# Performance work log

Measured on AMD Instinct MI355X. Metric: run time of the kernel, lower is better.

The kernel has to match this reference:

```python
import jax, jax.numpy as jnp
import numpy as np

T, B, DIM, N_STATE = 2048, 16, 1024, 1024
EPS = 1e-6


def setup_inputs() -> dict:
    key = jax.random.key(0)
    kx, kk, kv, kq = jax.random.split(key, 4)
    xavier = np.sqrt(2.0 / (N_STATE + DIM)).astype(np.float32)
    return {
        "x": jax.random.normal(kx, (T, B, DIM), dtype=jnp.float32),
        "W_k": jax.random.normal(kk, (N_STATE, DIM), dtype=jnp.float32) * xavier,
        "W_v": jax.random.normal(kv, (N_STATE, DIM), dtype=jnp.float32) * xavier,
        "W_q": jax.random.normal(kq, (N_STATE, DIM), dtype=jnp.float32) * xavier,
    }


def reference(x, W_k, W_v, W_q):
    # Projections for all timesteps at once: [T, B, n]
    k = jnp.einsum("tbd,nd->tbn", x, W_k)
    v = jnp.einsum("tbd,nd->tbn", x, W_v)
    q = jnp.einsum("tbd,nd->tbn", x, W_q)
    # L2-normalize k per (t, b) over the state dim (matches k_t.norm(dim=-1))
    k_norm = k / (jnp.linalg.norm(k, axis=-1, keepdims=True) + EPS)

    Tn, Bn, n = k.shape
    S0 = jnp.zeros((Bn, n), dtype=x.dtype)

    def step(S, inp):
        k_t, v_t, q_t = inp
        # Delta update with OUTPUT gating + tanh nonlinearity
        S_new = jnp.tanh(S * (1.0 - k_t * k_t) + v_t * k_t)
        Sq = S_new * q_t
        out = Sq * jax.nn.silu(Sq)
        return S_new, out

    S_final, output = jax.lax.scan(step, S0, (k_norm, v, q))
    return output, S_final
```

## Files before the change

### kernel.cpp

```cpp
#include <hip/hip_runtime.h>
#include <hip/hip_fp16.h>

#define T_STEPS 2048
#define BATCH 16
#define DIMD 1024
#define NSTATE 1024
#define MROWS (T_STEPS * BATCH)
#define NCH (BATCH * NSTATE)

typedef _Float16 f16x8 __attribute__((ext_vector_type(8)));
typedef float f32x4 __attribute__((ext_vector_type(4)));

#define GAS(p) ((const __attribute__((address_space(1))) void*)(p))
#define LAS(p) ((__attribute__((address_space(3))) void*)(p))

__global__ void cvt_kernel(const float* __restrict__ src, _Float16* __restrict__ dst, int n8) {
  int i = blockIdx.x * blockDim.x + threadIdx.x;
  if (i >= n8) return;
  const float4* s4 = (const float4*)src;
  float4 a = s4[(size_t)i * 2];
  float4 b = s4[(size_t)i * 2 + 1];
  f16x8 o;
  o[0] = (_Float16)a.x; o[1] = (_Float16)a.y; o[2] = (_Float16)a.z; o[3] = (_Float16)a.w;
  o[4] = (_Float16)b.x; o[5] = (_Float16)b.y; o[6] = (_Float16)b.z; o[7] = (_Float16)b.w;
  *((f16x8*)dst + i) = o;
}

__global__ void cvtW_kernel(const float* __restrict__ wk, const float* __restrict__ wv,
                            const float* __restrict__ wq, _Float16* __restrict__ dst) {
  const float* src = blockIdx.y == 0 ? wk : blockIdx.y == 1 ? wv : wq;
  int i = blockIdx.x * blockDim.x + threadIdx.x;
  const float4* s4 = (const float4*)src;
  float4 a = s4[(size_t)i * 2];
  float4 b = s4[(size_t)i * 2 + 1];
  f16x8 o;
  o[0] = (_Float16)a.x; o[1] = (_Float16)a.y; o[2] = (_Float16)a.z; o[3] = (_Float16)a.w;
  o[4] = (_Float16)b.x; o[5] = (_Float16)b.y; o[6] = (_Float16)b.z; o[7] = (_Float16)b.w;
  *((f16x8*)dst + (size_t)blockIdx.y * (NSTATE * DIMD / 8) + i) = o;
}

__global__ __launch_bounds__(512, 1) void gemm_kernel(const _Float16* __restrict__ A,
                                                      const _Float16* __restrict__ Wcat,
                                                      _Float16* __restrict__ KVQt,
                                                      float* __restrict__ rnpart) {
  __shared__ _Float16 lds[65536];
  const int tid = threadIdx.x;
  const int lane = tid & 63;
  const int w = tid >> 6;
  const int wm = w >> 2;
  const int wn = w & 3;

  const int bid = blockIdx.x;
  const int swz = (bid & 7) * 192 + (bid >> 3);
  const int mat = swz >> 9;
  const int rem = swz & 511;
  const int tileM = rem >> 2;
  const int tileN = rem & 3;

  const _Float16* Ag = A + (size_t)tileM * 256 * DIMD;
  const _Float16* Bg = Wcat + (size_t)mat * NSTATE * DIMD + (size_t)tileN * 256 * DIMD;

  const int s0 = tid, s1 = tid + 512;
  const int sr0 = s0 >> 2, sc0 = ((s0 & 3) ^ ((s0 >> 3) & 3)) * 8;
  const int sr1 = s1 >> 2, sc1 = ((s1 & 3) ^ ((s1 >> 3) & 3)) * 8;

#define STAGE_H(G, buf, reg, TT, h)                                                     \
  do {                                                                                  \
    __builtin_amdgcn_global_load_lds(                                                   \
        GAS(G + (size_t)sr0 * DIMD + (TT) * 64 + (h) * 32 + sc0),                       \
        LAS(lds + (buf) * 32768 + (reg) * 8192 + s0 * 8), 16, 0, 0);                    \
    __builtin_amdgcn_global_load_lds(                                                   \
        GAS(G + (size_t)sr1 * DIMD + (TT) * 64 + (h) * 32 + sc1),                       \
        LAS(lds + (buf) * 32768 + (reg) * 8192 + s1 * 8), 16, 0, 0);                    \
  } while (0)

  f32x4 acc[8][4];
#pragma unroll
  for (int m = 0; m < 8; ++m)
#pragma unroll
    for (int n = 0; n < 4; ++n)
      acc[m][n] = (f32x4){0.f, 0.f, 0.f, 0.f};

  STAGE_H(Ag, 0, 0, 0, 0);
  STAGE_H(Bg, 0, 2, 0, 0);
  STAGE_H(Ag, 0, 1, 0, 1);
  STAGE_H(Bg, 0, 3, 0, 1);

  const int fr = lane & 15;
  const int cbp = ((lane >> 4) ^ ((fr >> 1) & 3)) * 8;

#define KTILE(T)                                                                        \
  do {                                                                                  \
    const int buf = (T) & 1, bufn = buf ^ 1;                                            \
    f16x8 a0[8], b0[4], a1[8], b1[4];                                                   \
                 \
    asm volatile("s_waitcnt vmcnt(4)" ::: "memory");                                    \
    __builtin_amdgcn_s_barrier();                                                       \
    __builtin_amdgcn_sched_barrier(0);                                                  \
    if ((T) + 1 < 16) STAGE_H(Ag, bufn, 0, (T) + 1, 0);                                 \
    _Pragma("unroll") for (int m = 0; m < 8; ++m)                                       \
        a0[m] = *(const f16x8*)(lds + buf * 32768 + 0 * 8192 +                          \
                                (wm * 128 + m * 16 + fr) * 32 + cbp);                   \
    _Pragma("unroll") for (int n = 0; n < 4; ++n)                                       \
        b0[n] = *(const f16x8*)(lds + buf * 32768 + 2 * 8192 +                          \
                                (wn * 64 + n * 16 + fr) * 32 + cbp);                    \
    __builtin_amdgcn_s_setprio(1);                                                      \
    _Pragma("unroll") for (int m = 0; m < 8; ++m) _Pragma("unroll") for (int n = 0; n < 2; ++n) \
        acc[m][n] = __builtin_amdgcn_mfma_f32_16x16x32_f16(a0[m], b0[n], acc[m][n], 0, 0, 0); \
    __builtin_amdgcn_s_setprio(0);                                                      \
                                         \
    if ((T) + 1 < 16) STAGE_H(Bg, bufn, 2, (T) + 1, 0);                                 \
    __builtin_amdgcn_s_setprio(1);                                                      \
    _Pragma("unroll") for (int m = 0; m < 8; ++m) _Pragma("unroll") for (int n = 2; n < 4; ++n) \
        acc[m][n] = __builtin_amdgcn_mfma_f32_16x16x32_f16(a0[m], b0[n], acc[m][n], 0, 0, 0); \
    __builtin_amdgcn_s_setprio(0);                                                      \
                  \
    if ((T) + 1 < 16) {                                                                 \
      asm volatile("s_waitcnt vmcnt(4)" ::: "memory");                                  \
    } else {                                                                            \
      asm volatile("s_waitcnt vmcnt(0)" ::: "memory");                                  \
    }                                                                                   \
    __builtin_amdgcn_s_barrier();                                                       \
    __builtin_amdgcn_sched_barrier(0);                                                  \
    if ((T) + 1 < 16) STAGE_H(Ag, bufn, 1, (T) + 1, 1);                                 \
    _Pragma("unroll") for (int m = 0; m < 8; ++m)                                       \
        a1[m] = *(const f16x8*)(lds + buf * 32768 + 1 * 8192 +                          \
                                (wm * 128 + m * 16 + fr) * 32 + cbp);                   \
    _Pragma("unroll") for (int n = 0; n < 4; ++n)                                       \
        b1[n] = *(const f16x8*)(lds + buf * 32768 + 3 * 8192 +                          \
                                (wn * 64 + n * 16 + fr) * 32 + cbp);                    \
    __builtin_amdgcn_s_setprio(1);                                                      \
    _Pragma("unroll") for (int m = 0; m < 8; ++m) _Pragma("unroll") for (int n = 0; n < 2; ++n) \
        acc[m][n] = __builtin_amdgcn_mfma_f32_16x16x32_f16(a1[m], b1[n], acc[m][n], 0, 0, 0); \
    __builtin_amdgcn_s_setprio(0);                                                      \
                                         \
    if ((T) + 1 < 16) STAGE_H(Bg, bufn, 3, (T) + 1, 1);                                 \
    __builtin_amdgcn_s_setprio(1);                                                      \
    _Pragma("unroll") for (int m = 0; m < 8; ++m) _Pragma("unroll") for (int n = 2; n < 4; ++n) \
        acc[m][n] = __builtin_amdgcn_mfma_f32_16x16x32_f16(a1[m], b1[n], acc[m][n], 0, 0, 0); \
    __builtin_amdgcn_s_setprio(0);                                                      \
  } while (0)

  KTILE(0);  KTILE(1);  KTILE(2);  KTILE(3);
  KTILE(4);  KTILE(5);  KTILE(6);  KTILE(7);
  KTILE(8);  KTILE(9);  KTILE(10); KTILE(11);
  KTILE(12); KTILE(13); KTILE(14); KTILE(15);

  const int cc = lane & 15;
  const int l4 = lane >> 4;
  _Float16* Cb = KVQt + (size_t)mat * ((size_t)MROWS * NSTATE) +
                 (size_t)(tileM * 2 + wm) * ((size_t)NCH * 8);
#pragma unroll
  for (int n = 0; n < 4; ++n)
#pragma unroll
    for (int j = 0; j < 4; ++j) {
      f16x8 pk;
#pragma unroll
      for (int m = 0; m < 8; ++m) pk[m] = (_Float16)acc[m][n][j];
      const int b = l4 * 4 + j;
      const int gcol = tileN * 256 + wn * 64 + n * 16 + cc;
      *(f16x8*)(Cb + ((size_t)(b * 1024 + gcol)) * 8) = pk;
    }

  if (mat == 0) {
#pragma unroll
    for (int m = 0; m < 8; ++m)
#pragma unroll
      for (int j = 0; j < 4; ++j) {
        float p = 0.f;
#pragma unroll
        for (int n = 0; n < 4; ++n) p += acc[m][n][j] * acc[m][n][j];
        p += __shfl_xor(p, 1);
        p += __shfl_xor(p, 2);
        p += __shfl_xor(p, 4);
        p += __shfl_xor(p, 8);
        if (cc == 0) {
          const int gr = tileM * 256 + wm * 128 + m * 16 + l4 * 4 + j;
          rnpart[(size_t)(tileN * 4 + wn) * MROWS + gr] = p;
        }
      }
  }
}

__global__ void rnfin_kernel(const float* __restrict__ part, float* __restrict__ rnT) {
  const int r = blockIdx.x * 256 + threadIdx.x;
  float s = 0.f;
#pragma unroll
  for (int i = 0; i < 16; ++i) s += part[(size_t)i * MROWS + r];
  rnT[(r & 15) * T_STEPS + (r >> 4)] = 1.f / (sqrtf(s) + 1e-6f);
}

#define STILE 16

#define LOADT(P, t0in)                                                        \
  do {                                                                        \
    const int tc = ((t0in) < T_STEPS) ? (t0in) : (T_STEPS - STILE);           \
    const size_t o0 = ((size_t)(tc >> 3) * NCH + c) * 8;                      \
    P##k0 = *(const f16x8*)(Kt + o0);                                         \
    P##k1 = *(const f16x8*)(Kt + o0 + (size_t)NCH * 8);                       \
    P##v0 = *(const f16x8*)(Vt + o0);                                         \
    P##v1 = *(const f16x8*)(Vt + o0 + (size_t)NCH * 8);                       \
    P##q0 = *(const f16x8*)(Qt + o0);                                         \
    P##q1 = *(const f16x8*)(Qt + o0 + (size_t)NCH * 8);                       \
    P##r0 = *(const f32x4*)(rnT + bb + tc);                                   \
    P##r1 = *(const f32x4*)(rnT + bb + tc + 4);                               \
    P##r2 = *(const f32x4*)(rnT + bb + tc + 8);                               \
    P##r3 = *(const f32x4*)(rnT + bb + tc + 12);                              \
  } while (0)

#define STEPT(P, t0)                                                          \
  do {                                                                        \
    float a2[STILE], b2[STILE], qf[STILE];                                    \
    _Pragma("unroll") for (int i = 0; i < STILE; ++i) {                       \
      float kf = (float)((i < 8) ? P##k0[i & 7] : P##k1[i & 7]);              \
      float vf = (float)((i < 8) ? P##v0[i & 7] : P##v1[i & 7]);              \
      float rv = (i < 4) ? P##r0[i & 3]                                       \
               : (i < 8) ? P##r1[i & 3]                                       \
               : (i < 12) ? P##r2[i & 3] : P##r3[i & 3];                      \
      float kn = kf * rv;                                                     \
      a2[i] = L2E2 - (L2E2 * kn) * kn;                                        \
      b2[i] = L2E2 * (vf * kn);                                               \
      qf[i] = (float)((i < 8) ? P##q0[i & 7] : P##q1[i & 7]);                 \
    }                                                                         \
    _Pragma("unroll") for (int i = 0; i < STILE; ++i) {                       \
      float u = fmaf(S, a2[i], b2[i]);                                        \
      float e = __builtin_amdgcn_exp2f(u);                                    \
      float r = __builtin_amdgcn_rcpf(e + 1.f);                               \
      S = fmaf(-2.f, r, 1.f);                                                 \
      float z = S * qf[i];                                                    \
      float sg = __builtin_amdgcn_rcpf(1.f + __builtin_amdgcn_exp2f(-L2E * z)); \
      out[(size_t)((t0) + i) * NCH + c] = z * z * sg;                         \
    }                                                                         \
  } while (0)

__global__ __launch_bounds__(64) void scan_kernel(const _Float16* __restrict__ Kt,
                                                  const _Float16* __restrict__ Vt,
                                                  const _Float16* __restrict__ Qt,
                                                  const float* __restrict__ rnT,
                                                  float* __restrict__ out,
                                                  float* __restrict__ sfin) {
  const int c = blockIdx.x * 64 + threadIdx.x;
  const int bb = (c >> 10) * T_STEPS;
  constexpr float L2E2 = 2.8853900817779268f;
  constexpr float L2E = 1.4426950408889634f;
  float S = 0.f;
  f16x8 Ak0, Ak1, Av0, Av1, Aq0, Aq1;
  f16x8 Bk0, Bk1, Bv0, Bv1, Bq0, Bq1;
  f16x8 Ck0, Ck1, Cv0, Cv1, Cq0, Cq1;
  f16x8 Dk0, Dk1, Dv0, Dv1, Dq0, Dq1;
  f32x4 Ar0, Ar1, Ar2, Ar3, Br0, Br1, Br2, Br3;
  f32x4 Cr0, Cr1, Cr2, Cr3, Dr0, Dr1, Dr2, Dr3;

  LOADT(A, 0);
  LOADT(B, STILE);
  LOADT(C, 2 * STILE);
  for (int t0 = 0; t0 < T_STEPS; t0 += 4 * STILE) {
    LOADT(D, t0 + 3 * STILE);
    STEPT(A, t0);
    LOADT(A, t0 + 4 * STILE);
    STEPT(B, t0 + STILE);
    LOADT(B, t0 + 5 * STILE);
    STEPT(C, t0 + 2 * STILE);
    LOADT(C, t0 + 6 * STILE);
    STEPT(D, t0 + 3 * STILE);
  }
  sfin[c] = S;
}

extern "C" void kernel_launch(void* const* d_in, const int* in_sizes, int n_in,
                              void* d_out, int out_size, void* d_ws, size_t ws_size,
                              hipStream_t stream) {
  const float* x = (const float*)d_in[0];
  const float* Wk = (const float*)d_in[1];
  const float* Wv = (const float*)d_in[2];
  const float* Wq = (const float*)d_in[3];

  char* ws = (char*)d_ws;
  _Float16* xh = (_Float16*)ws;
  _Float16* Wh = (_Float16*)(ws + 67108864ull);
  _Float16* KVQt = (_Float16*)(ws + 67108864ull + 6291456ull);
  float* rnpart = (float*)(ws + 67108864ull + 6291456ull + 201326592ull);
  float* rnT = (float*)(ws + 67108864ull + 6291456ull + 201326592ull + 2097152ull);

  int n8x = MROWS * DIMD / 8;
  cvt_kernel<<<(n8x + 255) / 256, 256, 0, stream>>>(x, xh, n8x);
  cvtW_kernel<<<dim3(NSTATE * DIMD / 8 / 256, 3), 256, 0, stream>>>(Wk, Wv, Wq, Wh);

  gemm_kernel<<<1536, 512, 0, stream>>>(xh, Wh, KVQt, rnpart);

  rnfin_kernel<<<MROWS / 256, 256, 0, stream>>>(rnpart, rnT);

  const _Float16* Kt = KVQt;
  const _Float16* Vt = KVQt + (size_t)MROWS * NSTATE;
  const _Float16* Qt = KVQt + 2ull * MROWS * NSTATE;
  float* outp = (float*)d_out;
  scan_kernel<<<NCH / 64, 64, 0, stream>>>(Kt, Vt, Qt, rnT, outp, outp + (size_t)MROWS * NSTATE);
}
```

Before: 382.1 us.

## Split scan step into recurrence chain and deferred output, shorten critical path

Each step's state recurrence is rewritten in terms of the sigmoid reciprocal r, using S = 1 - 2r. This folds the S computation into precomputed per-step coefficients (p2, m2) and removes one dependent op from the serial chain. The gated SiLU output for each tile is moved out of the chain and run one tile later, so its independent arithmetic and stores can interleave with the next tile's recurrence. The prefetch ring shrinks from four tile buffers to three, with a rebuilt prologue and epilogue. This lowers register pressure but leaves less lookahead on loads.

```diff
diff --git a/kernel.cpp b/kernel.cpp
--- a/kernel.cpp
+++ b/kernel.cpp
@@ -208,9 +208,9 @@
     P##r3 = *(const f32x4*)(rnT + bb + tc + 12);                              \
   } while (0)
 
-#define STEPT(P, t0)                                                          \
+#define CHAINT(P)                                                             \
   do {                                                                        \
-    float a2[STILE], b2[STILE], qf[STILE];                                    \
+    float p2[STILE], m2[STILE];                                               \
     _Pragma("unroll") for (int i = 0; i < STILE; ++i) {                       \
       float kf = (float)((i < 8) ? P##k0[i & 7] : P##k1[i & 7]);              \
       float vf = (float)((i < 8) ? P##v0[i & 7] : P##v1[i & 7]);              \
@@ -218,18 +218,28 @@
                : (i < 8) ? P##r1[i & 3]                                       \
                : (i < 12) ? P##r2[i & 3] : P##r3[i & 3];                      \
       float kn = kf * rv;                                                     \
-      a2[i] = L2E2 - (L2E2 * kn) * kn;                                        \
-      b2[i] = L2E2 * (vf * kn);                                               \
-      qf[i] = (float)((i < 8) ? P##q0[i & 7] : P##q1[i & 7]);                 \
+      float t = L2E2 * kn;                                                    \
+      float a2 = fmaf(-t, kn, L2E2);                                          \
+      float b2 = t * vf;                                                      \
+      p2[i] = a2 + b2;                                                        \
+      m2[i] = -2.f * a2;                                                      \
     }                                                                         \
     _Pragma("unroll") for (int i = 0; i < STILE; ++i) {                       \
-      float u = fmaf(S, a2[i], b2[i]);                                        \
+      float u = fmaf(m2[i], r, p2[i]);                                        \
       float e = __builtin_amdgcn_exp2f(u);                                    \
-      float r = __builtin_amdgcn_rcpf(e + 1.f);                               \
-      S = fmaf(-2.f, r, 1.f);                                                 \
-      float z = S * qf[i];                                                    \
-      float sg = __builtin_amdgcn_rcpf(1.f + __builtin_amdgcn_exp2f(-L2E * z)); \
-      out[(size_t)((t0) + i) * NCH + c] = z * z * sg;                         \
+      r = __builtin_amdgcn_rcpf(e + 1.f);                                     \
+      Sv##P[i] = fmaf(-2.f, r, 1.f);                                          \
+    }                                                                         \
+  } while (0)
+
+#define OUTT(P, t0)                                                           \
+  do {                                                                        \
+    _Pragma("unroll") for (int i = 0; i < STILE; ++i) {                       \
+      float qf = (float)((i < 8) ? P##q0[i & 7] : P##q1[i & 7]);              \
+      float z = Sv##P[i] * qf;                                                \
+      float e = __builtin_amdgcn_exp2f(-L2E * z);                             \
+      float sg = __builtin_amdgcn_rcpf(1.f + e);                              \
+      out[(size_t)((t0) + i) * NCH + c] = (z * z) * sg;                       \
     }                                                                         \
   } while (0)
 
@@ -243,28 +253,30 @@
   const int bb = (c >> 10) * T_STEPS;
   constexpr float L2E2 = 2.8853900817779268f;
   constexpr float L2E = 1.4426950408889634f;
-  float S = 0.f;
+  float r = 0.5f;
   f16x8 Ak0, Ak1, Av0, Av1, Aq0, Aq1;
   f16x8 Bk0, Bk1, Bv0, Bv1, Bq0, Bq1;
   f16x8 Ck0, Ck1, Cv0, Cv1, Cq0, Cq1;
-  f16x8 Dk0, Dk1, Dv0, Dv1, Dq0, Dq1;
-  f32x4 Ar0, Ar1, Ar2, Ar3, Br0, Br1, Br2, Br3;
-  f32x4 Cr0, Cr1, Cr2, Cr3, Dr0, Dr1, Dr2, Dr3;
+  f32x4 Ar0, Ar1, Ar2, Ar3, Br0, Br1, Br2, Br3, Cr0, Cr1, Cr2, Cr3;
+  float SvA[STILE], SvB[STILE], SvC[STILE];
 
   LOADT(A, 0);
   LOADT(B, STILE);
+  CHAINT(A);
   LOADT(C, 2 * STILE);
-  for (int t0 = 0; t0 < T_STEPS; t0 += 4 * STILE) {
-    LOADT(D, t0 + 3 * STILE);
-    STEPT(A, t0);
+  CHAINT(B);  OUTT(A, 0);
+  LOADT(A, 3 * STILE);
+
+  for (int t0 = 2 * STILE; t0 + 3 * STILE <= T_STEPS; t0 += 3 * STILE) {
+    CHAINT(C);  OUTT(B, t0 - STILE);
+    LOADT(B, t0 + 2 * STILE);
+    CHAINT(A);  OUTT(C, t0);
+    LOADT(C, t0 + 3 * STILE);
+    CHAINT(B);  OUTT(A, t0 + STILE);
     LOADT(A, t0 + 4 * STILE);
-    STEPT(B, t0 + STILE);
-    LOADT(B, t0 + 5 * STILE);
-    STEPT(C, t0 + 2 * STILE);
-    LOADT(C, t0 + 6 * STILE);
-    STEPT(D, t0 + 3 * STILE);
   }
-  sfin[c] = S;
+  OUTT(B, T_STEPS - STILE);
+  sfin[c] = fmaf(-2.f, r, 1.f);
 }
 
 extern "C" void kernel_launch(void* const* d_in, const int* in_sizes, int n_in,
```

Result: no change. 389.3 us (+1.9%).
